# Kernel tuning notes

Measured on AMD Instinct MI355X. Metric: run time of the kernel, lower is better.

## Reference

```python
import jax, jax.numpy as jnp
import numpy as np

B, T = 32, 4096
DIM_VECT, DIM_ATTN = 512, 256
DIM_ATTN_BID = 2 * DIM_ATTN  # flag_bid=True


def setup_inputs() -> dict:
    key = jax.random.key(0)
    k1, k2, k3, k4, k5, k6 = jax.random.split(key, 6)
    s = lambda fan_in: 1.0 / np.sqrt(fan_in)
    return {
        "vector": jax.random.normal(k1, (B, DIM_VECT), dtype=jnp.float32),
        "matrix": jax.random.normal(k2, (B, T, DIM_ATTN_BID), dtype=jnp.float32),
        "input_lengths": jax.random.randint(k3, (B,), 1, T + 1, dtype=jnp.int64),
        # nn.Linear weights are [out_features, in_features]
        "W_vec": jax.random.uniform(k4, (DIM_ATTN, DIM_VECT), jnp.float32, -s(DIM_VECT), s(DIM_VECT)),
        "W_mat": jax.random.uniform(k5, (DIM_ATTN, DIM_ATTN_BID), jnp.float32, -s(DIM_ATTN_BID), s(DIM_ATTN_BID)),
        "W_attn": jax.random.uniform(k6, (1, DIM_ATTN), jnp.float32, -s(DIM_ATTN), s(DIM_ATTN)),
    }


def reference(vector, matrix, input_lengths, W_vec, W_mat, W_attn):
    # vector: [B, Dv], matrix: [B, T, Dm], lengths: [B]
    t1 = jnp.einsum("bd,ad->ba", vector, W_vec)          # [B, A]
    t2 = jnp.einsum("btd,ad->bta", matrix, W_mat)        # [B, T, A]
    t3 = jax.nn.relu(t1[:, None, :] + t2)                # [B, T, A]
    logits = jnp.einsum("bta,oa->bt", t3, W_attn)        # [B, T] (o == 1 squeezed)
    # original subtracts the GLOBAL max over the whole logits tensor
    unnorm = jnp.exp(logits - logits.max())              # [B, T]
    mask = jnp.arange(matrix.shape[1])[None, :] < input_lengths[:, None]
    masked = unnorm * mask.astype(unnorm.dtype)
    attentions = masked / masked.sum(axis=1, keepdims=True)
    representations = jnp.einsum("btd,bt->bd", matrix, attentions)
    return representations, attentions
```

## Files before the change

### kernel.cpp

```cpp
#include <hip/hip_runtime.h>
#include <hip/hip_bf16.h>
#include <math.h>

#define B_SZ 32
#define T_SZ 4096
#define DV   512
#define DA   256
#define DK   512

typedef __attribute__((ext_vector_type(8))) __bf16 bf16x8;
typedef __attribute__((ext_vector_type(4))) __bf16 bf16x4;
typedef __attribute__((ext_vector_type(4))) float  f32x4;

__device__ inline int get_len(const int* __restrict__ p, int b) {
    return (p[1] == 0) ? p[2 * b] : p[b];
}

__global__ void conv_wmat_kernel(const float* __restrict__ w, __bf16* __restrict__ out) {
    int i = (blockIdx.x * 256 + threadIdx.x) * 4;
    float4 v = *(const float4*)(w + i);
    bf16x4 o;
    o[0] = (__bf16)v.x; o[1] = (__bf16)v.y; o[2] = (__bf16)v.z; o[3] = (__bf16)v.w;
    *(bf16x4*)(out + i) = o;
}

__global__ void t1_kernel(const float* __restrict__ vector, const float* __restrict__ wvec,
                          float* __restrict__ t1, float* __restrict__ rep) {
    int b = blockIdx.x, tid = threadIdx.x;
    __shared__ float sv[DV];
    sv[tid]       = vector[b * DV + tid];
    sv[tid + 256] = vector[b * DV + tid + 256];
    rep[b * DV + tid]       = 0.f;
    rep[b * DV + tid + 256] = 0.f;
    __syncthreads();
    const float4* w  = (const float4*)(wvec + (size_t)tid * DV);
    const float4* s4 = (const float4*)sv;
    float acc = 0.f;
#pragma unroll 8
    for (int k = 0; k < DV / 4; k++) {
        float4 wv = w[k]; float4 xv = s4[k];
        acc += wv.x * xv.x + wv.y * xv.y + wv.z * xv.z + wv.w * xv.w;
    }
    t1[b * DA + tid] = acc;
}

#define TM  64
#define BK  32
#define LDT 40

__global__ __launch_bounds__(256) void logits_kernel(
    const float* __restrict__ matrix, const __bf16* __restrict__ wmat,
    const float* __restrict__ t1, const float* __restrict__ wattn,
    const int* __restrict__ lens, float* __restrict__ logits) {
    int b  = blockIdx.y;
    int t0 = blockIdx.x * TM;
    int len = get_len(lens, b);
    if (t0 >= len) return;

    __shared__ __bf16 sA[TM][LDT];
    __shared__ __bf16 sB[DA][LDT];
    __shared__ float s_t1[DA];
    __shared__ float s_wa[DA];
    __shared__ float s_logit[TM];

    int tid = threadIdx.x;
    s_t1[tid] = t1[b * DA + tid];
    s_wa[tid] = wattn[tid];
    if (tid < TM) s_logit[tid] = 0.f;

    int wave = tid >> 6, lane = tid & 63;
    int col = lane & 15;
    int kq  = (lane >> 4) * 8;

    f32x4 acc[4][4];
    f32x4 zero = {0.f, 0.f, 0.f, 0.f};
#pragma unroll
    for (int i = 0; i < 4; i++)
#pragma unroll
        for (int j = 0; j < 4; j++) acc[i][j] = zero;

    const float*  Ab = matrix + ((size_t)b * T_SZ + t0) * DK;
    const __bf16* Bb = wmat + (size_t)tid * DK;
    int am = tid >> 2;
    int ak = (tid & 3) * 8;

    for (int k0 = 0; k0 < DK; k0 += BK) {
        __syncthreads();
        float4 a0 = *(const float4*)(Ab + (size_t)am * DK + k0 + ak);
        float4 a1 = *(const float4*)(Ab + (size_t)am * DK + k0 + ak + 4);
        bf16x8 av;
        av[0] = (__bf16)a0.x; av[1] = (__bf16)a0.y; av[2] = (__bf16)a0.z; av[3] = (__bf16)a0.w;
        av[4] = (__bf16)a1.x; av[5] = (__bf16)a1.y; av[6] = (__bf16)a1.z; av[7] = (__bf16)a1.w;
        *(bf16x8*)&sA[am][ak] = av;
        const uint4* bsrc = (const uint4*)(Bb + k0);
        uint4 b0 = bsrc[0], b1 = bsrc[1], b2 = bsrc[2], b3 = bsrc[3];
        *(uint4*)&sB[tid][0]  = b0;
        *(uint4*)&sB[tid][8]  = b1;
        *(uint4*)&sB[tid][16] = b2;
        *(uint4*)&sB[tid][24] = b3;
        __syncthreads();

        bf16x8 af[4], bfr[4];
#pragma unroll
        for (int mt = 0; mt < 4; mt++) af[mt]  = *(const bf16x8*)&sA[mt * 16 + col][kq];
#pragma unroll
        for (int nt = 0; nt < 4; nt++) bfr[nt] = *(const bf16x8*)&sB[wave * 64 + nt * 16 + col][kq];
#pragma unroll
        for (int mt = 0; mt < 4; mt++)
#pragma unroll
            for (int nt = 0; nt < 4; nt++)
                acc[mt][nt] = __builtin_amdgcn_mfma_f32_16x16x32_bf16(af[mt], bfr[nt], acc[mt][nt], 0, 0, 0);
    }

    int rg = lane >> 4;
#pragma unroll
    for (int mt = 0; mt < 4; mt++) {
#pragma unroll
        for (int r = 0; r < 4; r++) {
            float v = 0.f;
#pragma unroll
            for (int nt = 0; nt < 4; nt++) {
                int a = wave * 64 + nt * 16 + col;
                float x = acc[mt][nt][r] + s_t1[a];
                v += s_wa[a] * fmaxf(x, 0.f);
            }
#pragma unroll
            for (int off = 1; off < 16; off <<= 1) v += __shfl_xor(v, off, 64);
            if (col == 0) atomicAdd(&s_logit[mt * 16 + rg * 4 + r], v);
        }
    }
    __syncthreads();
    if (tid < TM) logits[(size_t)b * T_SZ + t0 + tid] = s_logit[tid];
}

__global__ void softmax_kernel(const int* __restrict__ lens, float* __restrict__ attn) {
    int b = blockIdx.x, tid = threadIdx.x;
    int len = get_len(lens, b);
    float* row = attn + (size_t)b * T_SZ;
    __shared__ float sred[4];

    float m = -1e30f;
    for (int t = tid; t < len; t += 256) m = fmaxf(m, row[t]);
#pragma unroll
    for (int off = 32; off; off >>= 1) m = fmaxf(m, __shfl_xor(m, off, 64));
    if ((tid & 63) == 0) sred[tid >> 6] = m;
    __syncthreads();
    m = fmaxf(fmaxf(sred[0], sred[1]), fmaxf(sred[2], sred[3]));
    __syncthreads();

    float s = 0.f;
    for (int t = tid; t < len; t += 256) s += __expf(row[t] - m);
#pragma unroll
    for (int off = 32; off; off >>= 1) s += __shfl_xor(s, off, 64);
    if ((tid & 63) == 0) sred[tid >> 6] = s;
    __syncthreads();
    s = sred[0] + sred[1] + sred[2] + sred[3];
    float inv = 1.f / s;

    for (int t = tid; t < T_SZ; t += 256) {
        float v = (t < len) ? __expf(row[t] - m) * inv : 0.f;
        row[t] = v;
    }
}

#define TC 256
__global__ void rep_kernel(const float* __restrict__ matrix, const float* __restrict__ attn,
                           const int* __restrict__ lens, float* __restrict__ rep) {
    int b = blockIdx.y, c = blockIdx.x, tid = threadIdx.x;
    int len = get_len(lens, b);
    int t0 = c * TC;
    if (t0 >= len) return;
    __shared__ float sa[TC];
    sa[tid] = attn[(size_t)b * T_SZ + t0 + tid];
    __syncthreads();
    int n = min(TC, len - t0);
    const float* M = matrix + ((size_t)b * T_SZ + t0) * DK;
    float ax = 0.f, ay = 0.f;
    int d = 2 * tid;
#pragma unroll 4
    for (int t = 0; t < n; t++) {
        float w = sa[t];
        float2 mv = *(const float2*)(M + (size_t)t * DK + d);
        ax = fmaf(w, mv.x, ax);
        ay = fmaf(w, mv.y, ay);
    }
    atomicAdd(&rep[b * DV + d], ax);
    atomicAdd(&rep[b * DV + d + 1], ay);
}

extern "C" void kernel_launch(void* const* d_in, const int* in_sizes, int n_in,
                              void* d_out, int out_size, void* d_ws, size_t ws_size,
                              hipStream_t stream) {
    const float* vector = (const float*)d_in[0];
    const float* matrix = (const float*)d_in[1];
    const int*   lens   = (const int*)d_in[2];
    const float* wvec   = (const float*)d_in[3];
    const float* wmat   = (const float*)d_in[4];
    const float* wattn  = (const float*)d_in[5];

    float* rep  = (float*)d_out;
    float* attn = rep + B_SZ * DV;

    float*  t1      = (float*)d_ws;
    __bf16* wmat_bf = (__bf16*)((char*)d_ws + 32768);

    conv_wmat_kernel<<<dim3((DA * DK) / (256 * 4)), 256, 0, stream>>>(wmat, wmat_bf);
    t1_kernel<<<dim3(B_SZ), 256, 0, stream>>>(vector, wvec, t1, rep);
    logits_kernel<<<dim3(T_SZ / TM, B_SZ), 256, 0, stream>>>(matrix, wmat_bf, t1, wattn, lens, attn);
    softmax_kernel<<<dim3(B_SZ), 256, 0, stream>>>(lens, attn);
    rep_kernel<<<dim3(T_SZ / TC, B_SZ), 256, 0, stream>>>(matrix, attn, lens, rep);
}
```

Baseline: 442.2 us.

## Load GEMM fragments directly from global with register prefetch; widen softmax block

The logits GEMM drops its LDS staging and barriers. Each lane loads its MFMA fragments straight from global memory and prefetches the next k-slice into registers. The softmax kernel uses 1024 threads and keeps the row in registers instead of re-reading it three times. The rep kernel uses smaller time chunks for more blocks, with a deeper unroll. The trade-off is that each wave now re-reads the shared A rows itself, with less coalesced access and more global traffic, in exchange for removing synchronisation.

```diff
diff --git a/kernel.cpp b/kernel.cpp
--- a/kernel.cpp
+++ b/kernel.cpp
@@ -44,9 +44,7 @@
     t1[b * DA + tid] = acc;
 }
 
-#define TM  64
-#define BK  32
-#define LDT 40
+#define TM 64
 
 __global__ __launch_bounds__(256) void logits_kernel(
     const float* __restrict__ matrix, const __bf16* __restrict__ wmat,
@@ -57,8 +55,6 @@
     int len = get_len(lens, b);
     if (t0 >= len) return;
 
-    __shared__ __bf16 sA[TM][LDT];
-    __shared__ __bf16 sB[DA][LDT];
     __shared__ float s_t1[DA];
     __shared__ float s_wa[DA];
     __shared__ float s_logit[TM];
@@ -67,10 +63,20 @@
     s_t1[tid] = t1[b * DA + tid];
     s_wa[tid] = wattn[tid];
     if (tid < TM) s_logit[tid] = 0.f;
+    __syncthreads();
 
     int wave = tid >> 6, lane = tid & 63;
-    int col = lane & 15;
-    int kq  = (lane >> 4) * 8;
+    int col  = lane & 15;
+    int koff = (lane >> 4) * 8;
+
+    const float*  Arow[4];
+    const __bf16* Brow[4];
+#pragma unroll
+    for (int mt = 0; mt < 4; mt++)
+        Arow[mt] = matrix + ((size_t)b * T_SZ + t0 + mt * 16 + col) * DK + koff;
+#pragma unroll
+    for (int nt = 0; nt < 4; nt++)
+        Brow[nt] = wmat + (size_t)(wave * 64 + nt * 16 + col) * DK + koff;
 
     f32x4 acc[4][4];
     f32x4 zero = {0.f, 0.f, 0.f, 0.f};
@@ -79,37 +85,46 @@
 #pragma unroll
         for (int j = 0; j < 4; j++) acc[i][j] = zero;
 
-    const float*  Ab = matrix + ((size_t)b * T_SZ + t0) * DK;
-    const __bf16* Bb = wmat + (size_t)tid * DK;
-    int am = tid >> 2;
-    int ak = (tid & 3) * 8;
-
-    for (int k0 = 0; k0 < DK; k0 += BK) {
-        __syncthreads();
-        float4 a0 = *(const float4*)(Ab + (size_t)am * DK + k0 + ak);
-        float4 a1 = *(const float4*)(Ab + (size_t)am * DK + k0 + ak + 4);
-        bf16x8 av;
-        av[0] = (__bf16)a0.x; av[1] = (__bf16)a0.y; av[2] = (__bf16)a0.z; av[3] = (__bf16)a0.w;
-        av[4] = (__bf16)a1.x; av[5] = (__bf16)a1.y; av[6] = (__bf16)a1.z; av[7] = (__bf16)a1.w;
-        *(bf16x8*)&sA[am][ak] = av;
-        const uint4* bsrc = (const uint4*)(Bb + k0);
-        uint4 b0 = bsrc[0], b1 = bsrc[1], b2 = bsrc[2], b3 = bsrc[3];
-        *(uint4*)&sB[tid][0]  = b0;
-        *(uint4*)&sB[tid][8]  = b1;
-        *(uint4*)&sB[tid][16] = b2;
-        *(uint4*)&sB[tid][24] = b3;
-        __syncthreads();
-
-        bf16x8 af[4], bfr[4];
-#pragma unroll
-        for (int mt = 0; mt < 4; mt++) af[mt]  = *(const bf16x8*)&sA[mt * 16 + col][kq];
-#pragma unroll
-        for (int nt = 0; nt < 4; nt++) bfr[nt] = *(const bf16x8*)&sB[wave * 64 + nt * 16 + col][kq];
+    float4 a0[4], a1[4];
+    uint4  bv[4];
+#pragma unroll
+    for (int mt = 0; mt < 4; mt++) {
+        a0[mt] = *(const float4*)(Arow[mt]);
+        a1[mt] = *(const float4*)(Arow[mt] + 4);
+    }
+#pragma unroll
+    for (int nt = 0; nt < 4; nt++) bv[nt] = *(const uint4*)(Brow[nt]);
+
+    for (int ks = 0; ks < DK / 32; ks++) {
+        bf16x8 af[4], bfb[4];
+#pragma unroll
+        for (int mt = 0; mt < 4; mt++) {
+            bf16x8 v;
+            v[0] = (__bf16)a0[mt].x; v[1] = (__bf16)a0[mt].y;
+            v[2] = (__bf16)a0[mt].z; v[3] = (__bf16)a0[mt].w;
+            v[4] = (__bf16)a1[mt].x; v[5] = (__bf16)a1[mt].y;
+            v[6] = (__bf16)a1[mt].z; v[7] = (__bf16)a1[mt].w;
+            af[mt] = v;
+        }
+#pragma unroll
+        for (int nt = 0; nt < 4; nt++) bfb[nt] = *(bf16x8*)&bv[nt];
+
+        if (ks < DK / 32 - 1) {
+            int k1 = (ks + 1) * 32;
+#pragma unroll
+            for (int mt = 0; mt < 4; mt++) {
+                a0[mt] = *(const float4*)(Arow[mt] + k1);
+                a1[mt] = *(const float4*)(Arow[mt] + k1 + 4);
+            }
+#pragma unroll
+            for (int nt = 0; nt < 4; nt++) bv[nt] = *(const uint4*)(Brow[nt] + k1);
+        }
+
 #pragma unroll
         for (int mt = 0; mt < 4; mt++)
 #pragma unroll
             for (int nt = 0; nt < 4; nt++)
-                acc[mt][nt] = __builtin_amdgcn_mfma_f32_16x16x32_bf16(af[mt], bfr[nt], acc[mt][nt], 0, 0, 0);
+                acc[mt][nt] = __builtin_amdgcn_mfma_f32_16x16x32_bf16(af[mt], bfb[nt], acc[mt][nt], 0, 0, 0);
     }
 
     int rg = lane >> 4;
@@ -133,37 +148,51 @@
     if (tid < TM) logits[(size_t)b * T_SZ + t0 + tid] = s_logit[tid];
 }
 
-__global__ void softmax_kernel(const int* __restrict__ lens, float* __restrict__ attn) {
+__global__ __launch_bounds__(1024) void softmax_kernel(const int* __restrict__ lens,
+                                                       float* __restrict__ attn) {
     int b = blockIdx.x, tid = threadIdx.x;
     int len = get_len(lens, b);
     float* row = attn + (size_t)b * T_SZ;
-    __shared__ float sred[4];
+    __shared__ float sred[16];
+
+    float r[4];
+#pragma unroll
+    for (int i = 0; i < 4; i++) r[i] = row[tid + i * 1024];
 
     float m = -1e30f;
-    for (int t = tid; t < len; t += 256) m = fmaxf(m, row[t]);
+#pragma unroll
+    for (int i = 0; i < 4; i++)
+        if (tid + i * 1024 < len) m = fmaxf(m, r[i]);
 #pragma unroll
     for (int off = 32; off; off >>= 1) m = fmaxf(m, __shfl_xor(m, off, 64));
     if ((tid & 63) == 0) sred[tid >> 6] = m;
     __syncthreads();
-    m = fmaxf(fmaxf(sred[0], sred[1]), fmaxf(sred[2], sred[3]));
-    __syncthreads();
-
+    m = sred[0];
+#pragma unroll
+    for (int i = 1; i < 16; i++) m = fmaxf(m, sred[i]);
+    __syncthreads();
+
+    float e[4];
     float s = 0.f;
-    for (int t = tid; t < len; t += 256) s += __expf(row[t] - m);
+#pragma unroll
+    for (int i = 0; i < 4; i++) {
+        e[i] = (tid + i * 1024 < len) ? __expf(r[i] - m) : 0.f;
+        s += e[i];
+    }
 #pragma unroll
     for (int off = 32; off; off >>= 1) s += __shfl_xor(s, off, 64);
     if ((tid & 63) == 0) sred[tid >> 6] = s;
     __syncthreads();
-    s = sred[0] + sred[1] + sred[2] + sred[3];
+    s = 0.f;
+#pragma unroll
+    for (int i = 0; i < 16; i++) s += sred[i];
     float inv = 1.f / s;
 
-    for (int t = tid; t < T_SZ; t += 256) {
-        float v = (t < len) ? __expf(row[t] - m) * inv : 0.f;
-        row[t] = v;
-    }
-}
-
-#define TC 256
+#pragma unroll
+    for (int i = 0; i < 4; i++) row[tid + i * 1024] = e[i] * inv;
+}
+
+#define TC 128
 __global__ void rep_kernel(const float* __restrict__ matrix, const float* __restrict__ attn,
                            const int* __restrict__ lens, float* __restrict__ rep) {
     int b = blockIdx.y, c = blockIdx.x, tid = threadIdx.x;
@@ -171,13 +200,13 @@
     int t0 = c * TC;
     if (t0 >= len) return;
     __shared__ float sa[TC];
-    sa[tid] = attn[(size_t)b * T_SZ + t0 + tid];
+    if (tid < TC) sa[tid] = attn[(size_t)b * T_SZ + t0 + tid];
     __syncthreads();
     int n = min(TC, len - t0);
     const float* M = matrix + ((size_t)b * T_SZ + t0) * DK;
     float ax = 0.f, ay = 0.f;
     int d = 2 * tid;
-#pragma unroll 4
+#pragma unroll 8
     for (int t = 0; t < n; t++) {
         float w = sa[t];
         float2 mv = *(const float2*)(M + (size_t)t * DK + d);
@@ -207,6 +236,6 @@
     conv_wmat_kernel<<<dim3((DA * DK) / (256 * 4)), 256, 0, stream>>>(wmat, wmat_bf);
     t1_kernel<<<dim3(B_SZ), 256, 0, stream>>>(vector, wvec, t1, rep);
     logits_kernel<<<dim3(T_SZ / TM, B_SZ), 256, 0, stream>>>(matrix, wmat_bf, t1, wattn, lens, attn);
-    softmax_kernel<<<dim3(B_SZ), 256, 0, stream>>>(lens, attn);
+    softmax_kernel<<<dim3(B_SZ), 1024, 0, stream>>>(lens, attn);
     rep_kernel<<<dim3(T_SZ / TC, B_SZ), 256, 0, stream>>>(matrix, attn, lens, rep);
 }
```

New measurement: 475.9 us. 1.08x slower.
